# Kernel tuning notes

Measured on AMD Instinct MI355X. Metric: run time of the kernel, lower is better.

Reference implementation:

```python
import jax, jax.numpy as jnp
import numpy as np

SEQ_LEN = 2048
NUM_HEADS = 16
DIM_EMB = 1024
DIM_HEAD = DIM_EMB // NUM_HEADS  # 64
DIM_K = DIM_EMB  # source scales by dim_k**-0.5 with dim_k defaulting to dim_emb
BASE = 10000
EPS = float(np.finfo(np.float32).eps)


def _rope_tables(seq_len, dim_head):
    idx = jnp.arange(seq_len, dtype=jnp.float32)
    scale = 1.0 / (BASE ** (jnp.arange(0, dim_head, 2, dtype=jnp.float32) / dim_head) + EPS)
    pos = jnp.outer(idx, scale)              # [S, dh/2]
    pos = jnp.concatenate([pos, pos], axis=-1)  # [S, dh]
    return jnp.cos(pos), jnp.sin(pos)


def _rotate_half(x):
    x1, x2 = x[..., : DIM_HEAD // 2], x[..., DIM_HEAD // 2 :]
    return jnp.concatenate([-x2, x1], axis=-1)


def _apply_rope(x, cos, sin):
    # x: [B, H, S, dh]; cos/sin: [S, dh]
    return x * cos[None, None] + _rotate_half(x) * sin[None, None]


def setup_inputs() -> dict:
    key = jax.random.key(0)
    k1, k2, k3 = jax.random.split(key, 3)
    x = jax.random.normal(k1, (2, SEQ_LEN, DIM_EMB), dtype=jnp.float32)
    Wqkv = jax.random.normal(k2, (DIM_EMB, 3 * DIM_EMB), dtype=jnp.float32) * 0.02
    Wout = jax.random.normal(k3, (DIM_EMB, DIM_EMB), dtype=jnp.float32) * 0.02
    return {"x": x, "Wqkv": Wqkv, "Wout": Wout}


def reference(x, Wqkv, Wout):
    B = x.shape[0]
    cos, sin = _rope_tables(SEQ_LEN, DIM_HEAD)
    qkv = x @ Wqkv  # [B, S, 3*E]
    q, k, v = jnp.split(qkv, 3, axis=-1)

    def to_heads(t):
        return t.reshape(B, SEQ_LEN, NUM_HEADS, DIM_HEAD).transpose(0, 2, 1, 3)

    q, k, v = to_heads(q), to_heads(k), to_heads(v)
    q = _apply_rope(q, cos, sin)
    k = _apply_rope(k, cos, sin)

    scores = jnp.einsum('bhsd,bhtd->bhst', q, k) * (DIM_K ** -0.5)
    causal_mask = jnp.triu(jnp.ones((SEQ_LEN, SEQ_LEN), dtype=bool), k=1)
    scores = jnp.where(causal_mask[None, None], -jnp.inf, scores)
    attn = jax.nn.softmax(scores, axis=-1)
    out = jnp.einsum('bhst,bhtd->bhsd', attn, v)
    out = out.transpose(0, 2, 1, 3).reshape(B, SEQ_LEN, DIM_EMB)
    return out @ Wout
```

## Files before the change

### kernel.cpp

```cpp
#include <hip/hip_runtime.h>

#define S_LEN 2048
#define NHEAD 16

using f32x4  = __attribute__((ext_vector_type(4))) float;
using f32x16 = __attribute__((ext_vector_type(16))) float;
using bf16x8 = __attribute__((ext_vector_type(8))) __bf16;

__device__ __forceinline__ unsigned short f2bf(float f) {
  union { float f; unsigned u; } v; v.f = f;
  unsigned r = v.u + 0x7FFFu + ((v.u >> 16) & 1u);
  return (unsigned short)(r >> 16);
}
__device__ __forceinline__ float bf2f(unsigned short h) {
  union { unsigned u; float f; } v; v.u = ((unsigned)h) << 16; return v.f;
}
__device__ __forceinline__ void unpack8(uint4 u, float x[8]) {
  x[0]=bf2f((unsigned short)(u.x&0xffff)); x[1]=bf2f((unsigned short)(u.x>>16));
  x[2]=bf2f((unsigned short)(u.y&0xffff)); x[3]=bf2f((unsigned short)(u.y>>16));
  x[4]=bf2f((unsigned short)(u.z&0xffff)); x[5]=bf2f((unsigned short)(u.z>>16));
  x[6]=bf2f((unsigned short)(u.w&0xffff)); x[7]=bf2f((unsigned short)(u.w>>16));
}
__device__ __forceinline__ uint4 pack8(const unsigned short o[8]) {
  uint4 u;
  u.x = (unsigned)o[0] | ((unsigned)o[1]<<16);
  u.y = (unsigned)o[2] | ((unsigned)o[3]<<16);
  u.z = (unsigned)o[4] | ((unsigned)o[5]<<16);
  u.w = (unsigned)o[6] | ((unsigned)o[7]<<16);
  return u;
}
__device__ __forceinline__ void gload16(const void* g, void* l) {
  __builtin_amdgcn_global_load_lds(
      (const __attribute__((address_space(1))) unsigned int*)g,
      (__attribute__((address_space(3))) unsigned int*)l, 16, 0, 0);
}
__device__ __forceinline__ float exp2_fast(float x) {
#if __has_builtin(__builtin_amdgcn_exp2f)
  return __builtin_amdgcn_exp2f(x);
#else
  return __expf(x * 0.6931471805599453f);
#endif
}
__device__ __forceinline__ void store_c(float* C, size_t off, float v) { C[off] = v; }
__device__ __forceinline__ void store_c(unsigned short* C, size_t off, float v) { C[off] = f2bf(v); }

__global__ __launch_bounds__(256) void k_cvt(const float* __restrict__ in,
                                             unsigned short* __restrict__ out, int n8) {
  int i = blockIdx.x * 256 + threadIdx.x;
  if (i >= n8) return;
  const float4* p = (const float4*)in + 2 * (size_t)i;
  float4 a = p[0], b = p[1];
  unsigned short o[8] = { f2bf(a.x), f2bf(a.y), f2bf(a.z), f2bf(a.w),
                          f2bf(b.x), f2bf(b.y), f2bf(b.z), f2bf(b.w) };
  ((uint4*)out)[i] = pack8(o);
}

__global__ __launch_bounds__(256) void k_transpose_cvt(const float* __restrict__ in,
                                                       unsigned short* __restrict__ out,
                                                       int R, int C) {
  __shared__ float T[64][65];
  int r0 = blockIdx.x * 64, c0 = blockIdx.y * 64;
  int tid = threadIdx.x;
#pragma unroll
  for (int i = 0; i < 16; ++i) {
    int idx = tid + i * 256;
    int r = idx >> 6, c = idx & 63;
    T[r][c] = in[(size_t)(r0 + r) * C + c0 + c];
  }
  __syncthreads();
#pragma unroll
  for (int i = 0; i < 8; ++i) {
    int idx = tid + i * 256;
    int co = idx >> 5, rp = (idx & 31) * 2;
    unsigned v = (unsigned)f2bf(T[rp][co]) | ((unsigned)f2bf(T[rp + 1][co]) << 16);
    *(unsigned*)&out[(size_t)(c0 + co) * R + r0 + rp] = v;
  }
}

template <typename OUT_T>
__global__ __launch_bounds__(256) void k_gemm_bt(const unsigned short* __restrict__ A,
                                                 const unsigned short* __restrict__ Bt,
                                                 OUT_T* __restrict__ C,
                                                 int M, int N, int K) {
  __shared__ unsigned short As[128 * 32];
  __shared__ unsigned short Bs[128 * 32];
  int m0 = blockIdx.x * 128, n0 = blockIdx.y * 128;
  int tid = threadIdx.x;
  int lane = tid & 63, w = tid >> 6;
  int wr = w >> 1, wc = w & 1;
  int li = lane & 15, g = lane >> 4;

  const unsigned short* a_s0 = A + (size_t)(m0 + (tid >> 2)) * K + (tid & 3) * 8;
  const unsigned short* a_s1 = A + (size_t)(m0 + 64 + (tid >> 2)) * K + (tid & 3) * 8;
  const unsigned short* b_s0 = Bt + (size_t)(n0 + (tid >> 2)) * K + (tid & 3) * 8;
  const unsigned short* b_s1 = Bt + (size_t)(n0 + 64 + (tid >> 2)) * K + (tid & 3) * 8;
  unsigned short* As_d0 = &As[(w * 64) * 8];
  unsigned short* As_d1 = &As[(256 + w * 64) * 8];
  unsigned short* Bs_d0 = &Bs[(w * 64) * 8];
  unsigned short* Bs_d1 = &Bs[(256 + w * 64) * 8];

  f32x4 acc[4][4];
#pragma unroll
  for (int i = 0; i < 4; ++i)
#pragma unroll
    for (int j = 0; j < 4; ++j) acc[i][j] = (f32x4){0.f, 0.f, 0.f, 0.f};

  int nk = K >> 5;
  for (int kt = 0; kt < nk; ++kt) {
    int k0 = kt << 5;
    gload16(a_s0 + k0, As_d0);
    gload16(a_s1 + k0, As_d1);
    gload16(b_s0 + k0, Bs_d0);
    gload16(b_s1 + k0, Bs_d1);
    __syncthreads();
    bf16x8 af[4], bfr[4];
#pragma unroll
    for (int i = 0; i < 4; ++i)
      af[i] = *(const bf16x8*)&As[(wr * 64 + i * 16 + li) * 32 + g * 8];
#pragma unroll
    for (int j = 0; j < 4; ++j)
      bfr[j] = *(const bf16x8*)&Bs[(wc * 64 + j * 16 + li) * 32 + g * 8];
#pragma unroll
    for (int i = 0; i < 4; ++i)
#pragma unroll
      for (int j = 0; j < 4; ++j)
        acc[i][j] = __builtin_amdgcn_mfma_f32_16x16x32_bf16(af[i], bfr[j], acc[i][j], 0, 0, 0);
    __syncthreads();
  }
#pragma unroll
  for (int i = 0; i < 4; ++i) {
    int row = m0 + wr * 64 + i * 16 + g * 4;
#pragma unroll
    for (int j = 0; j < 4; ++j) {
      int col = n0 + wc * 64 + j * 16 + li;
#pragma unroll
      for (int r = 0; r < 4; ++r) store_c(C, (size_t)(row + r) * N + col, acc[i][j][r]);
    }
  }
}

__global__ __launch_bounds__(256) void k_rope_split(const unsigned short* __restrict__ qkv,
                                                    unsigned short* __restrict__ Qf,
                                                    unsigned short* __restrict__ Kf,
                                                    unsigned short* __restrict__ Vf) {
  int blk = blockIdx.x;
  int st = blk & 31, h = (blk >> 5) & 15, b = blk >> 9;
  int s0 = st * 64;
  int tid = threadIdx.x;
  int sl = tid >> 2, quad = tid & 3;
  int s = s0 + sl;
  int bh = b * NHEAD + h;
  int l31 = s & 31;
  int qt = s >> 5;
  int cq = quad >> 1, hiq = quad & 1;

  float cs[8], sn[8];
#pragma unroll
  for (int j = 0; j < 8; ++j) {
    int pr = quad * 8 + j;
    float freq = 1.0f / (powf(10000.0f, (float)pr * (1.0f / 32.0f)) + 1.1920928955078125e-07f);
    float ang = (float)s * freq;
    sincosf(ang, &sn[j], &cs[j]);
  }
  const unsigned short* row = qkv + (size_t)(b * S_LEN + s) * 3072;
  const float QSC = 0.04508422f;
  {
    float x1[8], x2[8];
    unpack8(*(const uint4*)&row[h * 64 + quad * 8], x1);
    unpack8(*(const uint4*)&row[h * 64 + 32 + quad * 8], x2);
    unsigned short o1[8], o2[8];
#pragma unroll
    for (int j = 0; j < 8; ++j) {
      o1[j] = f2bf((x1[j] * cs[j] - x2[j] * sn[j]) * QSC);
      o2[j] = f2bf((x2[j] * cs[j] + x1[j] * sn[j]) * QSC);
    }
    size_t base = ((size_t)bh * 64 + qt) * 4;
    int lane8 = (hiq * 32 + l31) * 8;
    *(uint4*)&Qf[(base + cq) * 512 + lane8] = pack8(o1);
    *(uint4*)&Qf[(base + 2 + cq) * 512 + lane8] = pack8(o2);
  }
  {
    float x1[8], x2[8];
    unpack8(*(const uint4*)&row[1024 + h * 64 + quad * 8], x1);
    unpack8(*(const uint4*)&row[1024 + h * 64 + 32 + quad * 8], x2);
    unsigned short o1[8], o2[8];
#pragma unroll
    for (int j = 0; j < 8; ++j) {
      o1[j] = f2bf(x1[j] * cs[j] - x2[j] * sn[j]);
      o2[j] = f2bf(x2[j] * cs[j] + x1[j] * sn[j]);
    }
    int lp = (l31 & 0x13) | ((l31 & 4) << 1) | ((l31 & 8) >> 1);
    size_t base = ((size_t)bh * 64 + qt) * 4;
    int lane8 = (hiq * 32 + lp) * 8;
    *(uint4*)&Kf[(base + cq) * 512 + lane8] = pack8(o1);
    *(uint4*)&Kf[(base + 2 + cq) * 512 + lane8] = pack8(o2);
  }
  __shared__ unsigned short Vl[64 * 72];
#pragma unroll
  for (int i = 0; i < 2; ++i) {
    int c = tid + i * 256;
    int r = c >> 3, c8 = (c & 7) * 8;
    *(uint4*)&Vl[r * 72 + c8] =
        *(const uint4*)&qkv[(size_t)(b * S_LEN + s0 + r) * 3072 + 2048 + h * 64 + c8];
  }
  __syncthreads();
  int d = tid >> 2, sc4 = tid & 3;
  unsigned o[8];
#pragma unroll
  for (int jj = 0; jj < 8; ++jj) {
    int sidx = sc4 * 16 + jj * 2;
    o[jj] = (unsigned)Vl[sidx * 72 + d] | ((unsigned)Vl[(sidx + 1) * 72 + d] << 16);
  }
  {
    int t = st * 2 + (sc4 >> 1);
    int c = ((d >> 5) << 1) + (sc4 & 1);
    size_t base = (((size_t)bh * 64 + t) * 4 + c) * 512;
    *(uint4*)&Vf[base + (d & 31) * 8]        = make_uint4(o[0], o[1], o[2], o[3]);
    *(uint4*)&Vf[base + (32 + (d & 31)) * 8] = make_uint4(o[4], o[5], o[6], o[7]);
  }
}

__global__ __launch_bounds__(256) void k_attn4(const unsigned short* __restrict__ Qf,
                                               const unsigned short* __restrict__ Kf,
                                               const unsigned short* __restrict__ Vf,
                                               unsigned short* __restrict__ O) {
  __shared__ float MBUF[4][2176];
  int bid = blockIdx.x;
  int i = (bid & 7) * 256 + (bid >> 3);
  int bh = i >> 6;
  int qt = 63 - (i & 63);
  int tid = threadIdx.x, w = tid >> 6, lane = tid & 63;
  int b = bh >> 4, h = bh & 15;
  int l31 = lane & 31, hi = lane >> 5;

  int n = qt + 1;
  int t0 = (w * n) >> 2, t1 = ((w + 1) * n) >> 2;

  const unsigned short* Kg = Kf + ((size_t)bh * 64) * 4 * 512 + lane * 8;
  const unsigned short* Vg = Vf + ((size_t)bh * 64) * 4 * 512 + lane * 8;

  float m_run = -1e30f, l_run = 0.f;
  f32x16 acc0, acc1;
#pragma unroll
  for (int r = 0; r < 16; ++r) { acc0[r] = 0.f; acc1[r] = 0.f; }

  if (t0 < t1) {
    const unsigned short* Qg = Qf + (((size_t)bh * 64 + qt) * 4) * 512 + lane * 8;
    bf16x8 qf[4];
#pragma unroll
    for (int c = 0; c < 4; ++c) qf[c] = *(const bf16x8*)(Qg + c * 512);

    auto loadK = [&](bf16x8 (&kf)[4], int t) {
      const unsigned short* kp = Kg + (size_t)t * 2048;
#pragma unroll
      for (int c = 0; c < 4; ++c) kf[c] = *(const bf16x8*)(kp + c * 512);
    };
    auto loadV = [&](bf16x8 (&vf)[4], int t) {
      const unsigned short* vp = Vg + (size_t)t * 2048;
#pragma unroll
      for (int c = 0; c < 4; ++c) vf[c] = *(const bf16x8*)(vp + c * 512);
    };
    auto step = [&](bf16x8 (&kf)[4], bf16x8 (&vf)[4], int t) {
      f32x16 s;
#pragma unroll
      for (int r = 0; r < 16; ++r) s[r] = 0.f;
      __builtin_amdgcn_s_setprio(1);
      s = __builtin_amdgcn_mfma_f32_32x32x16_bf16(kf[0], qf[0], s, 0, 0, 0);
      s = __builtin_amdgcn_mfma_f32_32x32x16_bf16(kf[1], qf[1], s, 0, 0, 0);
      s = __builtin_amdgcn_mfma_f32_32x32x16_bf16(kf[2], qf[2], s, 0, 0, 0);
      s = __builtin_amdgcn_mfma_f32_32x32x16_bf16(kf[3], qf[3], s, 0, 0, 0);
      __builtin_amdgcn_s_setprio(0);
      if (t == qt) {
#pragma unroll
        for (int r = 0; r < 16; ++r) {
          int kv = (r & 7) + 16 * (r >> 3) + 8 * hi;
          if (kv > l31) s[r] = -1e30f;
        }
      }
      float pmax;
      {
        float m0 = fmaxf(s[0], s[1]),   mm1 = fmaxf(s[2], s[3]);
        float m2 = fmaxf(s[4], s[5]),   m3 = fmaxf(s[6], s[7]);
        float m4 = fmaxf(s[8], s[9]),   m5 = fmaxf(s[10], s[11]);
        float m6 = fmaxf(s[12], s[13]), m7 = fmaxf(s[14], s[15]);
        m0 = fmaxf(m0, mm1); m2 = fmaxf(m2, m3); m4 = fmaxf(m4, m5); m6 = fmaxf(m6, m7);
        pmax = fmaxf(fmaxf(m0, m2), fmaxf(m4, m6));
      }
      if (__any(pmax > m_run + 8.0f)) {
        float pfull = fmaxf(pmax, __shfl_xor(pmax, 32));
        float mnew = fmaxf(m_run, pfull);
        float fac = exp2_fast(m_run - mnew);
        l_run *= fac;
#pragma unroll
        for (int r = 0; r < 16; ++r) { acc0[r] *= fac; acc1[r] *= fac; }
        m_run = mnew;
      }
#pragma unroll
      for (int r = 0; r < 16; ++r) s[r] = exp2_fast(s[r] - m_run);
      {
        float s0 = (s[0] + s[1]) + (s[2] + s[3]);
        float s1 = (s[4] + s[5]) + (s[6] + s[7]);
        float s2 = (s[8] + s[9]) + (s[10] + s[11]);
        float s3 = (s[12] + s[13]) + (s[14] + s[15]);
        l_run += (s0 + s1) + (s2 + s3);
      }
      bf16x8 pf0, pf1;
      {
        unsigned w0, w1, w2, w3;
        asm("v_cvt_pk_bf16_f32 %0, %1, %2" : "=v"(w0) : "v"(s[0]), "v"(s[1]));
        asm("v_cvt_pk_bf16_f32 %0, %1, %2" : "=v"(w1) : "v"(s[2]), "v"(s[3]));
        asm("v_cvt_pk_bf16_f32 %0, %1, %2" : "=v"(w2) : "v"(s[4]), "v"(s[5]));
        asm("v_cvt_pk_bf16_f32 %0, %1, %2" : "=v"(w3) : "v"(s[6]), "v"(s[7]));
        union { uint4 uu; bf16x8 v; } cv;
        cv.uu = make_uint4(w0, w1, w2, w3);
        pf0 = cv.v;
        asm("v_cvt_pk_bf16_f32 %0, %1, %2" : "=v"(w0) : "v"(s[8]), "v"(s[9]));
        asm("v_cvt_pk_bf16_f32 %0, %1, %2" : "=v"(w1) : "v"(s[10]), "v"(s[11]));
        asm("v_cvt_pk_bf16_f32 %0, %1, %2" : "=v"(w2) : "v"(s[12]), "v"(s[13]));
        asm("v_cvt_pk_bf16_f32 %0, %1, %2" : "=v"(w3) : "v"(s[14]), "v"(s[15]));
        cv.uu = make_uint4(w0, w1, w2, w3);
        pf1 = cv.v;
      }
      __builtin_amdgcn_s_setprio(1);
      acc0 = __builtin_amdgcn_mfma_f32_32x32x16_bf16(vf[0], pf0, acc0, 0, 0, 0);
      acc0 = __builtin_amdgcn_mfma_f32_32x32x16_bf16(vf[1], pf1, acc0, 0, 0, 0);
      acc1 = __builtin_amdgcn_mfma_f32_32x32x16_bf16(vf[2], pf0, acc1, 0, 0, 0);
      acc1 = __builtin_amdgcn_mfma_f32_32x32x16_bf16(vf[3], pf1, acc1, 0, 0, 0);
      __builtin_amdgcn_s_setprio(0);
    };

    bf16x8 kA[4], vA[4], kB[4], vB[4];
    loadK(kA, t0); loadV(vA, t0);
    int t = t0;
    while (true) {
      if (t + 1 < t1) { loadK(kB, t + 1); loadV(vB, t + 1); }
      step(kA, vA, t);
      ++t; if (t >= t1) break;
      if (t + 1 < t1) { loadK(kA, t + 1); loadV(vA, t + 1); }
      step(kB, vB, t);
      ++t; if (t >= t1) break;
    }
  }

  if (w != 0) {
    float* sb = &MBUF[w][0];
#pragma unroll
    for (int r = 0; r < 16; ++r) {
      sb[r * 64 + lane] = acc0[r];
      sb[(16 + r) * 64 + lane] = acc1[r];
    }
    sb[2048 + lane] = m_run;
    sb[2112 + lane] = l_run;
  }
  __syncthreads();
  if (w == 0) {
    float m1 = MBUF[1][2048 + lane], m2 = MBUF[2][2048 + lane], m3 = MBUF[3][2048 + lane];
    float mF = fmaxf(fmaxf(m_run, m1), fmaxf(m2, m3));
    float f0 = exp2_fast(m_run - mF);
    float f1 = exp2_fast(m1 - mF);
    float f2 = exp2_fast(m2 - mF);
    float f3 = exp2_fast(m3 - mF);
    float lF = f0 * l_run + f1 * MBUF[1][2112 + lane] + f2 * MBUF[2][2112 + lane] +
               f3 * MBUF[3][2112 + lane];
    lF += __shfl_xor(lF, 32);
    float inv = 1.0f / lF;
    f32x16 o0, o1;
#pragma unroll
    for (int r = 0; r < 16; ++r) {
      o0[r] = (f0 * acc0[r] + f1 * MBUF[1][r * 64 + lane] + f2 * MBUF[2][r * 64 + lane] +
               f3 * MBUF[3][r * 64 + lane]) * inv;
      o1[r] = (f0 * acc1[r] + f1 * MBUF[1][(16 + r) * 64 + lane] +
               f2 * MBUF[2][(16 + r) * 64 + lane] + f3 * MBUF[3][(16 + r) * 64 + lane]) * inv;
    }
    unsigned short* ol = (unsigned short*)&MBUF[0][0];
#pragma unroll
    for (int dh = 0; dh < 2; ++dh) {
#pragma unroll
      for (int r = 0; r < 16; r += 2) {
        int dv = dh * 32 + (r & 3) + 8 * (r >> 2) + 4 * hi;
        float lo = dh ? o1[r] : o0[r];
        float hi_ = dh ? o1[r + 1] : o0[r + 1];
        unsigned uu;
        asm("v_cvt_pk_bf16_f32 %0, %1, %2" : "=v"(uu) : "v"(lo), "v"(hi_));
        *(unsigned*)&ol[l31 * 72 + dv] = uu;
      }
    }
    asm volatile("s_waitcnt lgkmcnt(0)" ::: "memory");
    int q0f = qt * 32;
    int q = lane >> 1, half = lane & 1;
    unsigned short* op = O + ((size_t)(b * S_LEN + q0f + q)) * 1024 + h * 64 + half * 32;
#pragma unroll
    for (int j = 0; j < 4; ++j)
      *(uint4*)(op + j * 8) = *(const uint4*)&ol[q * 72 + half * 32 + j * 8];
  }
}

extern "C" void kernel_launch(void* const* d_in, const int* in_sizes, int n_in,
                              void* d_out, int out_size, void* d_ws, size_t ws_size,
                              hipStream_t stream) {
  const float* x = (const float*)d_in[0];
  const float* Wqkv = (const float*)d_in[1];
  const float* Wout = (const float*)d_in[2];
  float* out = (float*)d_out;
  char* ws = (char*)d_ws;
  unsigned short* xb = (unsigned short*)(ws);
  unsigned short* WqkvT = (unsigned short*)(ws + ((size_t)8 << 20));
  unsigned short* WoutT = (unsigned short*)(ws + ((size_t)14 << 20));
  unsigned short* qkv = (unsigned short*)(ws + ((size_t)16 << 20));
  unsigned short* Qf = (unsigned short*)(ws + ((size_t)40 << 20));
  unsigned short* Kf = (unsigned short*)(ws + ((size_t)48 << 20));
  unsigned short* Vf = (unsigned short*)(ws + ((size_t)56 << 20));

  k_cvt<<<2048, 256, 0, stream>>>(x, xb, 4096 * 1024 / 8);
  k_transpose_cvt<<<dim3(16, 48), 256, 0, stream>>>(Wqkv, WqkvT, 1024, 3072);
  k_transpose_cvt<<<dim3(16, 16), 256, 0, stream>>>(Wout, WoutT, 1024, 1024);
  k_gemm_bt<unsigned short><<<dim3(32, 24), 256, 0, stream>>>(xb, WqkvT, qkv, 4096, 3072, 1024);
  k_rope_split<<<1024, 256, 0, stream>>>(qkv, Qf, Kf, Vf);
  k_attn4<<<2048, 256, 0, stream>>>(Qf, Kf, Vf, xb );
  k_gemm_bt<float><<<dim3(32, 8), 256, 0, stream>>>(xb, WoutT, out, 4096, 1024, 1024);
}
```

Baseline: 134.8 us.

## Add 256x256 double-buffered QKV GEMM and faster RoPE trig

Replaces the 128x128 QKV projection GEMM with a new 512-thread kernel. It uses 256x256 output tiles, a K-step of 64, double-buffered LDS filled by direct global-to-LDS loads with explicit vmcnt waits, and raised MFMA priority. This is meant to improve data reuse and overlap loads with compute. The grid shrinks to 192 blocks, fewer than the CU count, and the unswizzled LDS rows may cause bank conflicts. Separately, the RoPE kernel swaps powf and sincosf for exp2, range reduction and __sinf/__cosf, which trades some accuracy for cheaper transcendental math.

```diff
diff --git a/kernel.cpp b/kernel.cpp
--- a/kernel.cpp
+++ b/kernel.cpp
@@ -135,6 +135,91 @@
       int col = n0 + wc * 64 + j * 16 + li;
 #pragma unroll
       for (int r = 0; r < 4; ++r) store_c(C, (size_t)(row + r) * N + col, acc[i][j][r]);
+    }
+  }
+}
+
+__global__ __launch_bounds__(512, 2) void k_gemm8(const unsigned short* __restrict__ A,
+                                                  const unsigned short* __restrict__ Bt,
+                                                  unsigned short* __restrict__ C,
+                                                  int M, int N, int K) {
+  __shared__ unsigned short As[2][256][64];
+  __shared__ unsigned short Bs[2][256][64];
+  const int tid = threadIdx.x;
+  const int lane = tid & 63, w = tid >> 6;
+  const int wm = w >> 2, wn = w & 3;
+  const int li = lane & 15, g = lane >> 4;
+  const int m0 = blockIdx.x * 256, n0 = blockIdx.y * 256;
+  const int srow = w * 8 + (lane >> 3);
+  const int scol = (lane & 7) * 8;
+
+  f32x4 acc[8][4];
+#pragma unroll
+  for (int i = 0; i < 8; ++i)
+#pragma unroll
+    for (int j = 0; j < 4; ++j) acc[i][j] = (f32x4){0.f, 0.f, 0.f, 0.f};
+
+  const int nt = K >> 6;
+
+  auto stage_tile = [&](int kt) {
+    int buf = kt & 1;
+    const unsigned short* sa = A + (size_t)(m0 + srow) * K + kt * 64 + scol;
+    const unsigned short* sb = Bt + (size_t)(n0 + srow) * K + kt * 64 + scol;
+    char* da = (char*)&As[buf][0][0] + w * 1024;
+    char* db = (char*)&Bs[buf][0][0] + w * 1024;
+    gload16(sa, da);
+    gload16(sa + (size_t)64 * K, da + 8192);
+    gload16(sa + (size_t)128 * K, da + 16384);
+    gload16(sa + (size_t)192 * K, da + 24576);
+    gload16(sb, db);
+    gload16(sb + (size_t)64 * K, db + 8192);
+    gload16(sb + (size_t)128 * K, db + 16384);
+    gload16(sb + (size_t)192 * K, db + 24576);
+  };
+
+  stage_tile(0);
+
+  for (int i = 0; i < nt; ++i) {
+    if (i + 1 < nt) {
+      stage_tile(i + 1);
+      asm volatile("s_waitcnt vmcnt(8)" ::: "memory");
+    } else {
+      asm volatile("s_waitcnt vmcnt(0)" ::: "memory");
+    }
+    __builtin_amdgcn_s_barrier();
+    asm volatile("" ::: "memory");
+    const int buf = i & 1;
+#pragma unroll
+    for (int kk = 0; kk < 2; ++kk) {
+      bf16x8 af[8], bfv[4];
+#pragma unroll
+      for (int ii = 0; ii < 8; ++ii)
+        af[ii] = *(const bf16x8*)&As[buf][wm * 128 + ii * 16 + li][kk * 32 + g * 8];
+#pragma unroll
+      for (int jj = 0; jj < 4; ++jj)
+        bfv[jj] = *(const bf16x8*)&Bs[buf][wn * 64 + jj * 16 + li][kk * 32 + g * 8];
+      __builtin_amdgcn_s_setprio(1);
+#pragma unroll
+      for (int ii = 0; ii < 8; ++ii)
+#pragma unroll
+        for (int jj = 0; jj < 4; ++jj)
+          acc[ii][jj] = __builtin_amdgcn_mfma_f32_16x16x32_bf16(af[ii], bfv[jj],
+                                                                acc[ii][jj], 0, 0, 0);
+      __builtin_amdgcn_s_setprio(0);
+    }
+    asm volatile("" ::: "memory");
+    __builtin_amdgcn_s_barrier();
+    asm volatile("" ::: "memory");
+  }
+
+#pragma unroll
+  for (int ii = 0; ii < 8; ++ii) {
+    int row = m0 + wm * 128 + ii * 16 + g * 4;
+#pragma unroll
+    for (int jj = 0; jj < 4; ++jj) {
+      int col = n0 + wn * 64 + jj * 16 + li;
+#pragma unroll
+      for (int r = 0; r < 4; ++r) C[(size_t)(row + r) * N + col] = f2bf(acc[ii][jj][r]);
     }
   }
 }
@@ -158,9 +243,13 @@
 #pragma unroll
   for (int j = 0; j < 8; ++j) {
     int pr = quad * 8 + j;
-    float freq = 1.0f / (powf(10000.0f, (float)pr * (1.0f / 32.0f)) + 1.1920928955078125e-07f);
-    float ang = (float)s * freq;
-    sincosf(ang, &sn[j], &cs[j]);
+    float e2 = exp2_fast((float)pr * 0.41524101f);
+    float freq = 1.0f / (e2 + 1.1920928955078125e-07f);
+    float x = (float)s * freq * 0.15915494309189535f;
+    x -= floorf(x);
+    float ang = x * 6.283185307179586f;
+    sn[j] = __sinf(ang);
+    cs[j] = __cosf(ang);
   }
   const unsigned short* row = qkv + (size_t)(b * S_LEN + s) * 3072;
   const float QSC = 0.04508422f;
@@ -414,7 +503,7 @@
   k_cvt<<<2048, 256, 0, stream>>>(x, xb, 4096 * 1024 / 8);
   k_transpose_cvt<<<dim3(16, 48), 256, 0, stream>>>(Wqkv, WqkvT, 1024, 3072);
   k_transpose_cvt<<<dim3(16, 16), 256, 0, stream>>>(Wout, WoutT, 1024, 1024);
-  k_gemm_bt<unsigned short><<<dim3(32, 24), 256, 0, stream>>>(xb, WqkvT, qkv, 4096, 3072, 1024);
+  k_gemm8<<<dim3(16, 12), 512, 0, stream>>>(xb, WqkvT, qkv, 4096, 3072, 1024);
   k_rope_split<<<1024, 256, 0, stream>>>(qkv, Qf, Kf, Vf);
   k_attn4<<<2048, 256, 0, stream>>>(Qf, Kf, Vf, xb );
   k_gemm_bt<float><<<dim3(32, 8), 256, 0, stream>>>(xb, WoutT, out, 4096, 1024, 1024);
```

New measurement: 137.2 us. About the same (+1.8%).
